# Optimization experiments

Measured on AMD Instinct MI355X. Metric: run time of the kernel, lower is better.

The kernel has to match this reference:

```python
import jax, jax.numpy as jnp
import numpy as np

N = 8192       # nodes
NHID = 128     # hidden dim (init kwarg nhid)
E = 262144     # edges (avg degree 32)
K = 64         # mean_kwargs k
TEMP = 1.0     # mean_kwargs temperature


def setup_inputs() -> dict:
    key = jax.random.key(0)
    k1, k2, k3 = jax.random.split(key, 3)
    x = jax.random.normal(k1, (N, NHID), jnp.float32)
    edge_index = jax.random.randint(k2, (2, E), 0, N, jnp.int32)
    W = jax.random.normal(k3, (NHID, NHID), jnp.float32) / np.sqrt(NHID)
    b = jnp.zeros((NHID,), jnp.float32)
    return {"x": x, "edge_index": edge_index, "W": W, "b": b}


def _gcn_adjacency(edge_index, n):
    # GCNConv normalization: add self loops, then D^-1/2 A D^-1/2 with unit edge weights.
    loops = jnp.arange(n, dtype=edge_index.dtype)
    row = jnp.concatenate([edge_index[0], loops])
    col = jnp.concatenate([edge_index[1], loops])
    w = jnp.ones(row.shape[0], jnp.float32)
    deg = jnp.zeros(n, jnp.float32).at[col].add(w)
    dinv = jnp.where(deg > 0, 1.0 / jnp.sqrt(deg), 0.0)
    norm = dinv[row] * w * dinv[col]
    # dense normalized adjacency (coalesced: duplicate edges summed, as torch.sparse coalesce does)
    return jnp.zeros((n, n), jnp.float32).at[row, col].add(norm)


def _soft_k_medoid(A, h, k=K, temperature=TEMP):
    # Soft weighted medoid over each node's top-k (by edge weight) neighborhood,
    # with weight correction (Geisler et al., 'Reliable GNNs via Robust Aggregation').
    n, d = h.shape
    row_sum = A.sum(-1, keepdims=True)                      # [n,1] (>0: self loops)
    tk_w, tk_idx = jax.lax.top_k(A, k)                      # [n,k]
    x_k = h[tk_idx]                                         # [n,k,d] neighbor gather
    # pairwise L2 distances within each neighborhood via the (a-b)^2 expansion
    sq = jnp.sum(x_k * x_k, -1)                             # [n,k]
    d2 = sq[:, :, None] + sq[:, None, :] - 2.0 * jnp.einsum('nkd,nmd->nkm', x_k, x_k)
    dist = jnp.sqrt(jnp.maximum(d2, 1e-12))                 # [n,k,k]
    # weighted total distance of each candidate j to the neighborhood
    l = jnp.einsum('nm,njm->nj', tk_w, dist)                # [n,k]
    l = jnp.where(tk_w > 0, l, jnp.inf)                     # padded slots get zero softmax mass
    s = jax.nn.softmax(-l / (temperature * row_sum), axis=-1)
    c = s * tk_w                                            # weight correction
    c = c / jnp.sum(c, -1, keepdims=True)
    return row_sum * jnp.einsum('nk,nkd->nd', c, x_k)       # [n,d]


def reference(x, edge_index, W, b):
    A = _gcn_adjacency(edge_index, x.shape[0])
    h = x @ W                                               # GCNConv linear (no bias)
    out = _soft_k_medoid(A, h) + b                          # robust aggregation + conv bias
    out = jax.nn.relu(out)
    # dropout is identity in eval mode
    return out @ out.T                                      # [n,n] reconstructed structure
```

## Files before the change

### kernel.cpp

```cpp
#include <hip/hip_runtime.h>
#include <hip/hip_bf16.h>
#include <math.h>

#define NN 8192
#define DD 128
#define EE 262144
#define CAPM 128

typedef __attribute__((ext_vector_type(8))) short bf16x8;
typedef __attribute__((ext_vector_type(4))) float f32x4;

__global__ __launch_bounds__(256) void k_init(int* deg, int* cnt) {
  int i = blockIdx.x * 256 + threadIdx.x;
  if (i < NN) { deg[i] = 1; cnt[i] = 0; }
}

__global__ __launch_bounds__(256) void k_scatter(const int* __restrict__ ei,
                                                 int* deg, int* cnt, int* bucket) {
  int e = blockIdx.x * 256 + threadIdx.x;
  if (e < EE) {
    int r = ei[e];
    int c = ei[EE + e];
    atomicAdd(&deg[c], 1);
    int pos = atomicAdd(&cnt[r], 1);
    if (pos < CAPM - 1) bucket[r * CAPM + pos] = c;
  }
}

__global__ __launch_bounds__(256) void k_dinv(const int* __restrict__ deg, float* dinv) {
  int i = blockIdx.x * 256 + threadIdx.x;
  if (i < NN) dinv[i] = 1.0f / sqrtf((float)deg[i]);
}

__global__ __launch_bounds__(256) void k_linear(const float* __restrict__ x,
                                                const float* __restrict__ W,
                                                float* __restrict__ h) {
  __shared__ float xr[2][DD];
  int j = threadIdx.x & 127, par = threadIdx.x >> 7;
  for (int rr = 0; rr < 16; rr += 2) {
    int row = blockIdx.x * 16 + rr + par;
    __syncthreads();
    xr[par][j] = x[row * DD + j];
    __syncthreads();
    float acc = 0.f;
    #pragma unroll 8
    for (int k = 0; k < DD; k++) acc = fmaf(xr[par][k], W[k * DD + j], acc);
    h[row * DD + j] = acc;
  }
}

#define XS 132
__global__ __launch_bounds__(256) void k_medoid(const int* __restrict__ cnt,
                                                const int* __restrict__ bucket,
                                                const float* __restrict__ dinv,
                                                const float* __restrict__ h,
                                                const float* __restrict__ bias,
                                                __hip_bfloat16* __restrict__ obf) {
  __shared__ int   sc[CAPM];
  __shared__ float sdv[CAPM];
  __shared__ float uw[CAPM];
  __shared__ int   uc[CAPM];
  __shared__ float Xk[64 * XS];
  __shared__ float sq[64];
  __shared__ float lv[64];
  __shared__ float carr[64];
  __shared__ float red[4];
  __shared__ int   s_wcnt[4];
  __shared__ float s_rs;
  __shared__ int   s_mu;

  const int r = blockIdx.x;
  const int tid = threadIdx.x;
  const int lane = tid & 63, wid = tid >> 6;

  const int cntr = min(cnt[r], CAPM - 1);
  const int m = cntr + 1;
  for (int p = tid; p < cntr; p += 256) sc[p] = bucket[r * CAPM + p];
  if (tid == 0) sc[cntr] = r;
  __syncthreads();
  const float dr = dinv[r];
  for (int p = tid; p < m; p += 256) sdv[p] = dinv[sc[p]];
  __syncthreads();

  bool head = false; int mult = 0; int c = -1; float dvp = 0.f;
  if (tid < m) {
    c = sc[tid]; dvp = sdv[tid];
    head = true;
    for (int q = 0; q < m; q++) {
      int cq = sc[q];
      if (cq == c) { mult++; if (q < tid) head = false; }
    }
  }

  float rpart = (tid < m) ? dvp : 0.f;
  for (int o = 32; o; o >>= 1) rpart += __shfl_xor(rpart, o);
  if (lane == 0) red[wid] = rpart;
  __syncthreads();
  if (tid == 0) s_rs = dr * (red[0] + red[1] + red[2] + red[3]);

  unsigned long long bal = __ballot(head);
  int rank = __popcll(bal & ((1ULL << lane) - 1ULL));
  if (lane == 0) s_wcnt[wid] = __popcll(bal);
  __syncthreads();
  int ubase = 0;
  for (int wq = 0; wq < wid; wq++) ubase += s_wcnt[wq];
  if (head) { int u = ubase + rank; uc[u] = c; uw[u] = (float)mult * dr * dvp; }
  if (tid == 0) s_mu = s_wcnt[0] + s_wcnt[1] + s_wcnt[2] + s_wcnt[3];
  __syncthreads();
  const int mu = s_mu;
  const float rs = s_rs;

  if (mu > 64) {
    for (int p = tid; p < CAPM; p += 256)
      if (p >= mu) { uw[p] = -1.f; uc[p] = 0x7fffffff; }
    __syncthreads();
    for (int kk = 2; kk <= CAPM; kk <<= 1) {
      for (int jj = kk >> 1; jj > 0; jj >>= 1) {
        if (tid < CAPM) {
          int ixj = tid ^ jj;
          if (ixj > tid) {
            float w1 = uw[tid], w2 = uw[ixj];
            int   c1 = uc[tid], c2 = uc[ixj];
            bool firstBefore = (w1 > w2) || (w1 == w2 && c1 < c2);
            bool up = ((tid & kk) == 0);
            bool sw = up ? !firstBefore : firstBefore;
            if (sw) { uw[tid] = w2; uw[ixj] = w1; uc[tid] = c2; uc[ixj] = c1; }
          }
        }
        __syncthreads();
      }
    }
  }
  __syncthreads();
  const int K = min(mu, 64);

  for (int t = tid; t < K * 32; t += 256) {
    int u = t >> 5, d4 = t & 31;
    float4 v = *(const float4*)(h + (size_t)uc[u] * DD + d4 * 4);
    *(float4*)(Xk + u * XS + d4 * 4) = v;
  }
  __syncthreads();

  {
    int u = tid >> 2, sub = tid & 3;
    if (u < 64) {
      float acc = 0.f;
      if (u < K) {
        for (int d4 = sub; d4 < 32; d4 += 4) {
          float4 v = *(const float4*)(Xk + u * XS + d4 * 4);
          acc += v.x * v.x + v.y * v.y + v.z * v.z + v.w * v.w;
        }
      }
      acc += __shfl_xor(acc, 1);
      acc += __shfl_xor(acc, 2);
      if (sub == 0 && u < K) sq[u] = acc;
    }
  }
  __syncthreads();

  {
    int j = tid >> 2, sub = tid & 3;
    float lacc = 0.f;
    if (j < K) {
      float sqj = sq[j];
      const float* A = Xk + j * XS;
      for (int mm = sub; mm < K; mm += 4) {
        const float* B = Xk + mm * XS;
        float dot = 0.f;
        #pragma unroll 8
        for (int d4 = 0; d4 < 32; d4++) {
          float4 a = *(const float4*)(A + d4 * 4);
          float4 bq = *(const float4*)(B + d4 * 4);
          dot = fmaf(a.x, bq.x, fmaf(a.y, bq.y, fmaf(a.z, bq.z, fmaf(a.w, bq.w, dot))));
        }
        float d2 = sqj + sq[mm] - 2.f * dot;
        float dist = sqrtf(fmaxf(d2, 1e-12f));
        lacc = fmaf(uw[mm], dist, lacc);
      }
    }
    lacc += __shfl_xor(lacc, 1);
    lacc += __shfl_xor(lacc, 2);
    if (j < K && (tid & 3) == 0) lv[j] = lacc;
  }
  __syncthreads();

  if (tid < 64) {
    float lj = (tid < K) ? lv[tid] : INFINITY;
    float z = -lj / rs;
    float zm = z;
    for (int o = 32; o; o >>= 1) zm = fmaxf(zm, __shfl_xor(zm, o));
    float e = (tid < K) ? expf(z - zm) : 0.f;
    float esum = e;
    for (int o = 32; o; o >>= 1) esum += __shfl_xor(esum, o);
    float s = e / esum;
    float cc = (tid < K) ? s * uw[tid] : 0.f;
    float csum = cc;
    for (int o = 32; o; o >>= 1) csum += __shfl_xor(csum, o);
    carr[tid] = cc / csum * rs;
  }
  __syncthreads();

  if (tid < DD) {
    int d = tid;
    float acc = 0.f;
    for (int j = 0; j < K; j++) acc = fmaf(carr[j], Xk[j * XS + d], acc);
    acc += bias[d];
    acc = fmaxf(acc, 0.f);
    obf[(size_t)r * DD + d] = __float2bfloat16(acc);
  }
}

__global__ __launch_bounds__(256) void k_outer(const short* __restrict__ ob,
                                               float* __restrict__ C) {
  const int lane = threadIdx.x & 63, w = threadIdx.x >> 6;
  const int R0 = blockIdx.x * 128 + (w >> 1) * 64;
  const int C0 = blockIdx.y * 128 + (w & 1) * 64;
  const int ra = lane & 15;
  const int kg = (lane >> 4) * 8;

  f32x4 acc[4][4] = {};
  #pragma unroll
  for (int ks = 0; ks < 4; ks++) {
    bf16x8 a[4], bb[4];
    #pragma unroll
    for (int f = 0; f < 4; f++) {
      a[f]  = *(const bf16x8*)(ob + (size_t)(R0 + f * 16 + ra) * DD + ks * 32 + kg);
      bb[f] = *(const bf16x8*)(ob + (size_t)(C0 + f * 16 + ra) * DD + ks * 32 + kg);
    }
    #pragma unroll
    for (int fi = 0; fi < 4; fi++)
      #pragma unroll
      for (int fj = 0; fj < 4; fj++)
        acc[fi][fj] = __builtin_amdgcn_mfma_f32_16x16x32_bf16(a[fi], bb[fj], acc[fi][fj], 0, 0, 0);
  }
  #pragma unroll
  for (int fi = 0; fi < 4; fi++) {
    int rbase = R0 + fi * 16 + (lane >> 4) * 4;
    #pragma unroll
    for (int reg = 0; reg < 4; reg++) {
      float* Crow = C + (size_t)(rbase + reg) * NN + (lane & 15);
      #pragma unroll
      for (int fj = 0; fj < 4; fj++)
        Crow[C0 + fj * 16] = acc[fi][fj][reg];
    }
  }
}

extern "C" void kernel_launch(void* const* d_in, const int* in_sizes, int n_in,
                              void* d_out, int out_size, void* d_ws, size_t ws_size,
                              hipStream_t stream) {
  const float* x  = (const float*)d_in[0];
  const int*   ei = (const int*)d_in[1];
  const float* W  = (const float*)d_in[2];
  const float* b  = (const float*)d_in[3];
  float* C = (float*)d_out;

  char* base = (char*)d_ws;
  int*   deg  = (int*)base;
  int*   cnt  = (int*)(base + 32 * 1024);
  float* dinv = (float*)(base + 64 * 1024);
  float* h    = (float*)(base + 96 * 1024);
  __hip_bfloat16* obf = (__hip_bfloat16*)(base + 96 * 1024 + 4 * 1024 * 1024);
  int*   bucket = (int*)(base + 96 * 1024 + 6 * 1024 * 1024);

  k_init   <<<NN / 256, 256, 0, stream>>>(deg, cnt);
  k_scatter<<<EE / 256, 256, 0, stream>>>(ei, deg, cnt, bucket);
  k_dinv   <<<NN / 256, 256, 0, stream>>>(deg, dinv);
  k_linear <<<NN / 16, 256, 0, stream>>>(x, W, h);
  k_medoid <<<NN, 256, 0, stream>>>(cnt, bucket, dinv, h, b, obf);
  k_outer  <<<dim3(64, 64), 256, 0, stream>>>((const short*)obf, C);
}
```

Measured before the change: 484.9 us.

## Register-tile pairwise distance with 4x4 blocks and symmetric upper-triangle computation

Replaces the per-row dot-product loop with 4x4 register tiles over the upper triangle of the KxK distance matrix. Each tile is computed once and its distances are added to both row and column sums through shared-memory atomics. This cuts LDS reads per FMA and halves the distance work by exploiting symmetry. In exchange only up to 136 threads are active, register use goes up, and shared atomics change the summation order.

```diff
diff --git a/kernel.cpp b/kernel.cpp
--- a/kernel.cpp
+++ b/kernel.cpp
@@ -134,6 +134,7 @@
   __syncthreads();
   const int K = min(mu, 64);
 
+  if (tid < 64) lv[tid] = 0.f;
   for (int t = tid; t < K * 32; t += 256) {
     int u = t >> 5, d4 = t & 31;
     float4 v = *(const float4*)(h + (size_t)uc[u] * DD + d4 * 4);
@@ -159,28 +160,67 @@
   __syncthreads();
 
   {
-    int j = tid >> 2, sub = tid & 3;
-    float lacc = 0.f;
-    if (j < K) {
-      float sqj = sq[j];
-      const float* A = Xk + j * XS;
-      for (int mm = sub; mm < K; mm += 4) {
-        const float* B = Xk + mm * XS;
-        float dot = 0.f;
-        #pragma unroll 8
-        for (int d4 = 0; d4 < 32; d4++) {
-          float4 a = *(const float4*)(A + d4 * 4);
-          float4 bq = *(const float4*)(B + d4 * 4);
-          dot = fmaf(a.x, bq.x, fmaf(a.y, bq.y, fmaf(a.z, bq.z, fmaf(a.w, bq.w, dot))));
+    const int ntile = (K + 3) >> 2;
+    const int T = ntile * (ntile + 1) / 2;
+    if (tid < T) {
+      int p = tid, ti = 0;
+      while (p >= ntile - ti) { p -= ntile - ti; ti++; }
+      int tj = ti + p;
+      const int j0 = ti * 4, m0 = tj * 4;
+      float dd[4][4];
+      #pragma unroll
+      for (int i = 0; i < 4; i++)
+        #pragma unroll
+        for (int jj = 0; jj < 4; jj++) dd[i][jj] = 0.f;
+      const float* Arow = Xk + j0 * XS;
+      const float* Brow = Xk + m0 * XS;
+      #pragma unroll 2
+      for (int d4 = 0; d4 < 32; d4++) {
+        float4 a0 = *(const float4*)(Arow + 0 * XS + d4 * 4);
+        float4 a1 = *(const float4*)(Arow + 1 * XS + d4 * 4);
+        float4 a2 = *(const float4*)(Arow + 2 * XS + d4 * 4);
+        float4 a3 = *(const float4*)(Arow + 3 * XS + d4 * 4);
+        float4 b0 = *(const float4*)(Brow + 0 * XS + d4 * 4);
+        float4 b1 = *(const float4*)(Brow + 1 * XS + d4 * 4);
+        float4 b2 = *(const float4*)(Brow + 2 * XS + d4 * 4);
+        float4 b3 = *(const float4*)(Brow + 3 * XS + d4 * 4);
+        #pragma unroll
+        for (int i = 0; i < 4; i++) {
+          float4 a = (i == 0) ? a0 : (i == 1) ? a1 : (i == 2) ? a2 : a3;
+          #pragma unroll
+          for (int jj = 0; jj < 4; jj++) {
+            float4 bq = (jj == 0) ? b0 : (jj == 1) ? b1 : (jj == 2) ? b2 : b3;
+            dd[i][jj] = fmaf(a.x, bq.x, fmaf(a.y, bq.y, fmaf(a.z, bq.z, fmaf(a.w, bq.w, dd[i][jj]))));
+          }
         }
-        float d2 = sqj + sq[mm] - 2.f * dot;
-        float dist = sqrtf(fmaxf(d2, 1e-12f));
-        lacc = fmaf(uw[mm], dist, lacc);
       }
-    }
-    lacc += __shfl_xor(lacc, 1);
-    lacc += __shfl_xor(lacc, 2);
-    if (j < K && (tid & 3) == 0) lv[j] = lacc;
+      float lpJ[4] = {0.f, 0.f, 0.f, 0.f};
+      float lpM[4] = {0.f, 0.f, 0.f, 0.f};
+      #pragma unroll
+      for (int i = 0; i < 4; i++) {
+        int j = j0 + i;
+        #pragma unroll
+        for (int jj = 0; jj < 4; jj++) {
+          int mc = m0 + jj;
+          if (j < K && mc < K && j <= mc) {
+            float d2 = sq[j] + sq[mc] - 2.f * dd[i][jj];
+            float dist = sqrtf(fmaxf(d2, 1e-12f));
+            if (j == mc) {
+              lpJ[i] += uw[j] * dist;
+            } else {
+              lpJ[i] += uw[mc] * dist;
+              lpM[jj] += uw[j] * dist;
+            }
+          }
+        }
+      }
+      #pragma unroll
+      for (int i = 0; i < 4; i++)
+        if (lpJ[i] != 0.f) atomicAdd(&lv[j0 + i], lpJ[i]);
+      #pragma unroll
+      for (int jj = 0; jj < 4; jj++)
+        if (lpM[jj] != 0.f) atomicAdd(&lv[m0 + jj], lpM[jj]);
+    }
   }
   __syncthreads();
 
```

Result: no change. 476.8 us (-1.7%).
